# Kernel optimization log

Hardware: AMD Instinct MI355X
Metric: run time of the kernel (lower is better)

## Reference

```python
import jax, jax.numpy as jnp
from jax import lax
import numpy as np

STRIDE = 16.0
PRE_NMS_TOPN = 2000
POST_NMS_TOPN = 300
NMS_THRESH = 0.7
BBOX_XFORM_CLIP = float(np.log(1000.0 / 16.0))
NUM_ANCHORS = 15

# ---- Detectron generate_anchors (numpy, done once) ----

def _whctrs(a):
    w = a[2] - a[0] + 1.0
    h = a[3] - a[1] + 1.0
    return w, h, a[0] + 0.5 * (w - 1), a[1] + 0.5 * (h - 1)

def _mkanchors(ws, hs, xc, yc):
    ws = ws[:, None]; hs = hs[:, None]
    return np.hstack([xc - 0.5 * (ws - 1), yc - 0.5 * (hs - 1),
                      xc + 0.5 * (ws - 1), yc + 0.5 * (hs - 1)])

def _ratio_enum(anchor, ratios):
    w, h, xc, yc = _whctrs(anchor)
    size = w * h
    ws = np.round(np.sqrt(size / ratios))
    hs = np.round(ws * ratios)
    return _mkanchors(ws, hs, xc, yc)

def _scale_enum(anchor, scales):
    w, h, xc, yc = _whctrs(anchor)
    return _mkanchors(w * scales, h * scales, xc, yc)

def generate_anchors(stride, sizes, ratios):
    base = np.array([1, 1, stride, stride], dtype=np.float64) - 1
    ra = _ratio_enum(base, np.asarray(ratios, np.float64))
    anchors = np.vstack([_scale_enum(ra[i], np.asarray(sizes, np.float64) / stride)
                         for i in range(ra.shape[0])])
    return anchors.astype(np.float32)

ANCHORS_NP = generate_anchors(STRIDE, (32, 64, 128, 256, 512), (0.5, 1.0, 2.0))

# ---- proposal helpers (jax) ----

def decode_boxes(anchors, deltas):
    w = anchors[:, 2] - anchors[:, 0] + 1.0
    h = anchors[:, 3] - anchors[:, 1] + 1.0
    cx = anchors[:, 0] + 0.5 * w
    cy = anchors[:, 1] + 0.5 * h
    dx, dy = deltas[:, 0], deltas[:, 1]
    dw = jnp.minimum(deltas[:, 2], BBOX_XFORM_CLIP)
    dh = jnp.minimum(deltas[:, 3], BBOX_XFORM_CLIP)
    pcx = dx * w + cx
    pcy = dy * h + cy
    pw = jnp.exp(dw) * w
    ph = jnp.exp(dh) * h
    return jnp.stack([pcx - 0.5 * pw, pcy - 0.5 * ph,
                      pcx + 0.5 * pw - 1.0, pcy + 0.5 * ph - 1.0], axis=-1)

def clip_boxes(b, info):
    hmax = info[0] - 1.0
    wmax = info[1] - 1.0
    return jnp.stack([jnp.clip(b[:, 0], 0.0, wmax), jnp.clip(b[:, 1], 0.0, hmax),
                      jnp.clip(b[:, 2], 0.0, wmax), jnp.clip(b[:, 3], 0.0, hmax)], axis=-1)

def nms_keep(boxes):
    # boxes already sorted by descending score; greedy NMS via scan
    x1, y1, x2, y2 = boxes[:, 0], boxes[:, 1], boxes[:, 2], boxes[:, 3]
    areas = (x2 - x1 + 1.0) * (y2 - y1 + 1.0)
    xx1 = jnp.maximum(x1[:, None], x1[None, :])
    yy1 = jnp.maximum(y1[:, None], y1[None, :])
    xx2 = jnp.minimum(x2[:, None], x2[None, :])
    yy2 = jnp.minimum(y2[:, None], y2[None, :])
    inter = jnp.maximum(xx2 - xx1 + 1.0, 0.0) * jnp.maximum(yy2 - yy1 + 1.0, 0.0)
    iou = inter / (areas[:, None] + areas[None, :] - inter)
    K = boxes.shape[0]

    def body(keep, i):
        sup = jnp.any(keep & (iou[i] > NMS_THRESH))
        keep = keep.at[i].set(~sup)
        return keep, None

    keep, _ = lax.scan(body, jnp.zeros((K,), bool), jnp.arange(K))
    return keep


def setup_inputs() -> dict:
    key = jax.random.key(0)
    ks = jax.random.split(key, 4)
    x = jax.random.normal(ks[0], (2, 1024, 50, 84), jnp.float32)
    conv_w = 0.01 * jax.random.normal(ks[1], (1024, 1024, 3, 3), jnp.float32)
    conv_b = jnp.zeros((1024,), jnp.float32)
    cls_w = 0.01 * jax.random.normal(ks[2], (2 * NUM_ANCHORS, 1024, 1, 1), jnp.float32)
    cls_b = jnp.zeros((2 * NUM_ANCHORS,), jnp.float32)
    bbox_w = 0.01 * jax.random.normal(ks[3], (4 * NUM_ANCHORS, 1024, 1, 1), jnp.float32)
    bbox_b = jnp.zeros((4 * NUM_ANCHORS,), jnp.float32)
    im_info = jnp.array([[800.0, 1344.0, 1.0], [800.0, 1344.0, 1.0]], jnp.float32)
    return {"x": x, "conv_w": conv_w, "conv_b": conv_b, "cls_w": cls_w,
            "cls_b": cls_b, "bbox_w": bbox_w, "bbox_b": bbox_b, "im_info": im_info}


def reference(x, conv_w, conv_b, cls_w, cls_b, bbox_w, bbox_b, im_info):
    A = NUM_ANCHORS
    anchors = jnp.asarray(ANCHORS_NP)
    dn = ('NCHW', 'OIHW', 'NCHW')
    h = jax.nn.relu(lax.conv_general_dilated(x, conv_w, (1, 1), 'SAME',
                                             dimension_numbers=dn) + conv_b[None, :, None, None])
    cls_logits = lax.conv_general_dilated(h, cls_w, (1, 1), 'VALID',
                                          dimension_numbers=dn) + cls_b[None, :, None, None]
    bbox_pred = lax.conv_general_dilated(h, bbox_w, (1, 1), 'VALID',
                                         dimension_numbers=dn) + bbox_b[None, :, None, None]
    B, _, H, W = cls_logits.shape
    # softmax over the 2-way fg/bg axis, take fg prob: [B, A, H, W]
    prob = jax.nn.softmax(cls_logits.reshape(B, 2, A, H, W), axis=1)[:, 1]
    scores = prob.transpose(0, 2, 3, 1).reshape(B, -1)               # [B, H*W*A]
    deltas = bbox_pred.transpose(0, 2, 3, 1).reshape(B, H * W * A, 4)
    # shifted anchor grid, (h, w, a) flatten order matching Detectron
    sy = jnp.arange(H, dtype=jnp.float32) * STRIDE
    sx = jnp.arange(W, dtype=jnp.float32) * STRIDE
    ys, xs = jnp.meshgrid(sy, sx, indexing='ij')
    shifts = jnp.stack([xs, ys, xs, ys], axis=-1).reshape(-1, 4)      # [H*W, 4]
    all_anchors = (shifts[:, None, :] + anchors[None, :, :]).reshape(-1, 4)

    def per_image(sc, dl, info):
        boxes = clip_boxes(decode_boxes(all_anchors, dl), info)
        top_sc, idx = lax.top_k(sc, PRE_NMS_TOPN)
        top_boxes = boxes[idx]
        keep = nms_keep(top_boxes)
        order = jnp.argsort((~keep).astype(jnp.int32))[:POST_NMS_TOPN]  # kept first, score order
        valid = keep[order]
        out_boxes = jnp.where(valid[:, None], top_boxes[order], 0.0)
        out_sc = jnp.where(valid, top_sc[order], 0.0)
        return out_boxes, out_sc

    rois_b, probs_b = jax.vmap(per_image)(scores, deltas, im_info)
    batch_ids = jnp.repeat(jnp.arange(B, dtype=jnp.float32), POST_NMS_TOPN)
    rois = jnp.concatenate([batch_ids[:, None], rois_b.reshape(-1, 4)], axis=1)
    return cls_logits, bbox_pred, rois, probs_b.reshape(-1, 1)
```

## Files before the change

kernel.cpp:

```cpp
#include <hip/hip_runtime.h>
#include <math.h>

#define BATCH   2
#define CIN     1024
#define COUT    1024
#define HH      50
#define WW      84
#define HWX     4200
#define NA      15
#define NSC     63000
#define TOPN    2000
#define POSTN   300
#define CAP     8192
#define CLS_OFF   0
#define BBOX_OFF  252000
#define ROIS_OFF  756000
#define PROBS_OFF 759000

#define TPI 273
#define USTR 274

__constant__ double ANCH[NA][4] = {
  {-15.0,  -4.0,  30.0, 19.0},
  {-38.0, -16.0,  53.0, 31.0},
  {-84.0, -40.0,  99.0, 55.0},
  {-176.0,-88.0, 191.0,103.0},
  {-360.0,-184.0,375.0,199.0},
  {-8.0,  -8.0,  23.0, 23.0},
  {-24.0, -24.0, 39.0, 39.0},
  {-56.0, -56.0, 71.0, 71.0},
  {-120.0,-120.0,135.0,135.0},
  {-248.0,-248.0,263.0,263.0},
  {-3.0, -14.0, 18.0, 29.0},
  {-14.0, -36.0, 29.0, 51.0},
  {-36.0, -80.0, 51.0, 95.0},
  {-80.0,-168.0, 95.0,183.0},
  {-168.0,-344.0,183.0,359.0}
};

__constant__ double BTd[6][6] = {
  {4.0,  0.0, -5.0,  0.0, 1.0, 0.0},
  {0.0, -4.0, -4.0,  1.0, 1.0, 0.0},
  {0.0,  4.0, -4.0, -1.0, 1.0, 0.0},
  {0.0, -2.0, -1.0,  2.0, 1.0, 0.0},
  {0.0,  2.0, -1.0, -2.0, 1.0, 0.0},
  {0.0,  4.0,  0.0, -5.0, 0.0, 1.0}
};
__constant__ double ATd[4][6] = {
  {1.0, 1.0,  1.0, 1.0,  1.0, 0.0},
  {0.0, 1.0, -1.0, 2.0, -2.0, 0.0},
  {0.0, 1.0,  1.0, 4.0,  4.0, 0.0},
  {0.0, 1.0, -1.0, 8.0, -8.0, 1.0}
};

#define BBOX_CLIP 4.1351665567423560

#define WS_WT     0
#define WS_U      98304
#define WS_V      3465216
#define WS_C      16048128
#define WS_H64    19402752
#define OV_H      WS_V
#define OV_SC     (WS_C + 0)
#define OV_TIDX   (WS_C + 126000)
#define OV_TSC    (WS_C + 130000)
#define OV_BOX    (WS_C + 134000)
#define OV_MASK   (WS_C + 166000)

typedef double dx4 __attribute__((ext_vector_type(4)));

__device__ __forceinline__ void gload16(const void* gptr, void* lptr) {
  __builtin_amdgcn_global_load_lds(
      (const __attribute__((address_space(1))) unsigned int*)gptr,
      (__attribute__((address_space(3))) unsigned int*)lptr, 16, 0, 0);
}
#define MFMA64(a, b, c) __builtin_amdgcn_mfma_f64_16x16x4f64(a, b, c, 0, 0, 0)

__launch_bounds__(256)
__global__ void itrans_k(const float* __restrict__ x, double* __restrict__ U,
                         int b, int r) {
  __shared__ float XT[8][6][84];
  const int bx = blockIdx.x;
  const int cg  = bx & 127;
  const int ty  = bx >> 7;
  const int ci0 = cg * 8;
  for (int e = threadIdx.x; e < 4032; e += 256) {
    int ci = e / 504, rem = e % 504;
    int ry = rem / 84, xx = rem % 84;
    int y = ty*4 - 1 + ry;
    float v = 0.f;
    if (y >= 0 && y < HH) v = x[((size_t)(b*CIN + ci0 + ci)*HH + y)*WW + xx];
    XT[ci][ry][xx] = v;
  }
  __syncthreads();
  const int tid = threadIdx.x;
  if (tid < 168) {
    const int ci = tid / 21, tx = tid % 21;
    const double c0 = BTd[r][0], c1 = BTd[r][1], c2 = BTd[r][2];
    const double c3 = BTd[r][3], c4 = BTd[r][4], c5 = BTd[r][5];
    double tt[6];
#pragma unroll
    for (int j = 0; j < 6; ++j) {
      int col = tx*4 - 1 + j;
      double v = 0.0;
      if (col >= 0 && col < WW) {
        v = c0*(double)XT[ci][0][col] + c1*(double)XT[ci][1][col]
          + c2*(double)XT[ci][2][col] + c3*(double)XT[ci][3][col]
          + c4*(double)XT[ci][4][col] + c5*(double)XT[ci][5][col];
      }
      tt[j] = v;
    }
    const int t = ty*21 + tx;
#pragma unroll
    for (int c = 0; c < 6; ++c) {
      double u = BTd[c][0]*tt[0] + BTd[c][1]*tt[1] + BTd[c][2]*tt[2]
               + BTd[c][3]*tt[3] + BTd[c][4]*tt[4] + BTd[c][5]*tt[5];
      U[(size_t)(c*1024 + ci0 + ci)*USTR + t] = u;
    }
  }
}

#define GR0(a,b,c) (0.25*(a))
#define GR1(a,b,c) (-((a)+(b)+(c))*(1.0/6.0))
#define GR2(a,b,c) ((-(a)+(b)-(c))*(1.0/6.0))
#define GR3(a,b,c) (((a)+2.0*(b)+4.0*(c))*(1.0/24.0))
#define GR4(a,b,c) (((a)-2.0*(b)+4.0*(c))*(1.0/24.0))
#define GR5(a,b,c) ((c))
__launch_bounds__(256)
__global__ void wtrans_k(const float* __restrict__ conv_w, double* __restrict__ V,
                         int r) {
  const int g = blockIdx.x*256 + threadIdx.x;
  const int co = g & 1023, ci = g >> 10;
  const float* gp = conv_w + (size_t)(co*1024 + ci)*9;
  double g00 = (double)gp[0], g01 = (double)gp[1], g02 = (double)gp[2];
  double g10 = (double)gp[3], g11 = (double)gp[4], g12 = (double)gp[5];
  double g20 = (double)gp[6], g21 = (double)gp[7], g22 = (double)gp[8];
  double p0, p1, p2;
  switch (r) {
    case 0: p0=GR0(g00,g10,g20); p1=GR0(g01,g11,g21); p2=GR0(g02,g12,g22); break;
    case 1: p0=GR1(g00,g10,g20); p1=GR1(g01,g11,g21); p2=GR1(g02,g12,g22); break;
    case 2: p0=GR2(g00,g10,g20); p1=GR2(g01,g11,g21); p2=GR2(g02,g12,g22); break;
    case 3: p0=GR3(g00,g10,g20); p1=GR3(g01,g11,g21); p2=GR3(g02,g12,g22); break;
    case 4: p0=GR4(g00,g10,g20); p1=GR4(g01,g11,g21); p2=GR4(g02,g12,g22); break;
    default:p0=GR5(g00,g10,g20); p1=GR5(g01,g11,g21); p2=GR5(g02,g12,g22); break;
  }
  const size_t cico = (size_t)ci*1024 + co;
  V[0ull*1048576ull + cico] = GR0(p0,p1,p2);
  V[1ull*1048576ull + cico] = GR1(p0,p1,p2);
  V[2ull*1048576ull + cico] = GR2(p0,p1,p2);
  V[3ull*1048576ull + cico] = GR3(p0,p1,p2);
  V[4ull*1048576ull + cico] = GR4(p0,p1,p2);
  V[5ull*1048576ull + cico] = GR5(p0,p1,p2);
}

__launch_bounds__(256, 2)
__global__ void wgemm_k(const double* __restrict__ U, const double* __restrict__ V,
                        double* __restrict__ C) {
  __shared__ __align__(16) double As[2][32*64];
  __shared__ __align__(16) double Bs[2][32*64];
  const int tid = threadIdx.x;
  const int lane = tid & 63;
  const int w = tid >> 6;
  const int wm = w >> 1, wn = w & 1;
  const int l15 = lane & 15, lq = lane >> 4;
  const int bx = blockIdx.x;
  const int mt = bx >> 4, nt = bx & 15;
  const int t0 = mt * 64, n0 = nt * 64;
  const int z = blockIdx.z;
  const double* Ub = U + (size_t)z * (1024ull*USTR);
  const double* Vb = V + (size_t)z * 1048576ull;
  double* Cb = C + (size_t)z * ((size_t)TPI*1024);

  int pidx[4], nidx[4];
  {
    dx4 pr = {0.,0.,0.,0.}, pc = {0.,0.,0.,0.};
    pr = MFMA64((double)l15, 1.0, pr);
    pc = MFMA64(1.0, (double)l15, pc);
#pragma unroll
    for (int i = 0; i < 4; ++i) {
      pidx[i] = ((int)pr[i]) >> 2;
      nidx[i] = ((int)pc[i]) >> 2;
    }
  }

  auto stage = [&](int k0s, int slot) {
    char* Ad = (char*)&As[slot][0];
    char* Bd = (char*)&Bs[slot][0];
#pragma unroll
    for (int i = 0; i < 4; ++i) {
      int u = tid + i*256;
      int row = u >> 5, cp = u & 31;
      int t = t0 + 2*cp; if (t > 272) t = 272;
      gload16(Ub + (size_t)(k0s + row)*USTR + t, Ad + u*16);
    }
#pragma unroll
    for (int i = 0; i < 4; ++i) {
      int u = tid + i*256;
      int row = u >> 5, cp = u & 31;
      gload16(Vb + (size_t)(k0s + row)*1024 + n0 + 2*cp, Bd + u*16);
    }
  };

  dx4 acc[2][2];
#pragma unroll
  for (int i = 0; i < 2; ++i)
#pragma unroll
    for (int j = 0; j < 2; ++j) acc[i][j] = (dx4){0.,0.,0.,0.};

  stage(0, 0);
  __syncthreads();
  int cur = 0;
#pragma unroll 1
  for (int k0 = 0; k0 < 1024; k0 += 32) {
    if (k0 + 32 < 1024) stage(k0 + 32, cur ^ 1);
    const double* Ap = &As[cur][0];
    const double* Bp = &Bs[cur][0];
#pragma unroll
    for (int kk = 0; kk < 32; kk += 4) {
      const int ar = (kk + lq)*64 + wm*32 + l15;
      double a0 = Ap[ar], a1 = Ap[ar + 16];
      const int br = (kk + lq)*64 + wn*32 + l15;
      double b0 = Bp[br], b1 = Bp[br + 16];
      acc[0][0] = MFMA64(a0, b0, acc[0][0]);
      acc[0][1] = MFMA64(a0, b1, acc[0][1]);
      acc[1][0] = MFMA64(a1, b0, acc[1][0]);
      acc[1][1] = MFMA64(a1, b1, acc[1][1]);
    }
    __syncthreads();
    cur ^= 1;
  }

#pragma unroll
  for (int m2 = 0; m2 < 2; ++m2) {
#pragma unroll
    for (int n2 = 0; n2 < 2; ++n2) {
#pragma unroll
      for (int i = 0; i < 4; ++i) {
        int t = t0 + wm*32 + m2*16 + pidx[i];
        int co = n0 + wn*32 + n2*16 + nidx[i];
        if (t < TPI) Cb[(size_t)t*1024 + co] = acc[m2][n2][i];
      }
    }
  }
}

__launch_bounds__(256)
__global__ void otrans_k(const double* __restrict__ C, double* __restrict__ h64b,
                         int r) {
  const int g = blockIdx.x*256 + threadIdx.x;
  const int co = g & 1023, t = g >> 10;
  double m0 = C[((size_t)0*TPI + t)*1024 + co];
  double m1 = C[((size_t)1*TPI + t)*1024 + co];
  double m2 = C[((size_t)2*TPI + t)*1024 + co];
  double m3 = C[((size_t)3*TPI + t)*1024 + co];
  double m4 = C[((size_t)4*TPI + t)*1024 + co];
  double m5 = C[((size_t)5*TPI + t)*1024 + co];
  double s[4];
#pragma unroll
  for (int bb = 0; bb < 4; ++bb)
    s[bb] = ATd[bb][0]*m0 + ATd[bb][1]*m1 + ATd[bb][2]*m2
          + ATd[bb][3]*m3 + ATd[bb][4]*m4 + ATd[bb][5]*m5;
  const int ty = t / 21, tx = t % 21;
#pragma unroll
  for (int a = 0; a < 4; ++a) {
    const int y = ty*4 + a;
    if (y >= HH) continue;
    const double fa = ATd[a][r];
#pragma unroll
    for (int bb = 0; bb < 4; ++bb) {
      const size_t idx = ((size_t)(y*WW + tx*4 + bb))*1024 + co;
      if (r == 0) h64b[idx] = fa * s[bb];
      else        h64b[idx] += fa * s[bb];
    }
  }
}

__launch_bounds__(256)
__global__ void fin_k(const double* __restrict__ h64, const float* __restrict__ bias,
                      float* __restrict__ h) {
  __shared__ float T[64*65];
  const int m0  = blockIdx.x * 64;
  const int co0 = blockIdx.y * 64;
  const int b   = blockIdx.z;
  const int tid = threadIdx.x;
#pragma unroll
  for (int i = 0; i < 16; ++i) {
    int e = tid + i*256;
    int mi = e >> 6, coi = e & 63;
    int m = m0 + mi;
    double v = 0.0;
    if (m < HWX) v = h64[((size_t)b*HWX + m)*1024 + co0 + coi];
    T[mi*65 + coi] = (float)fmax(v + (double)bias[co0 + coi], 0.0);
  }
  __syncthreads();
#pragma unroll
  for (int i = 0; i < 16; ++i) {
    int e = tid + i*256;
    int coi = e >> 6, mi = e & 63;
    int m = m0 + mi;
    if (m < HWX) h[((size_t)(b*COUT + co0 + coi))*HWX + m] = T[mi*65 + coi];
  }
}

__global__ void wt_k(const float* __restrict__ cls_w, const float* __restrict__ bbox_w,
                     float* __restrict__ wT) {
  int t = blockIdx.x*256 + threadIdx.x;
  if (t >= 96*1024) return;
  int c = t / 96, o = t - (t/96)*96;
  float v = 0.f;
  if (o < 30)      v = cls_w[(size_t)o*1024 + c];
  else if (o < 90) v = bbox_w[(size_t)(o-30)*1024 + c];
  wT[t] = v;
}

__launch_bounds__(256, 2)
__global__ void heads_k(const float* __restrict__ h, const float* __restrict__ wT,
                        const float* __restrict__ cls_b, const float* __restrict__ bbox_b,
                        float* __restrict__ out_cls, float* __restrict__ out_bbox) {
  __shared__ __align__(16) float As[2][32*32];
  __shared__ __align__(16) float Bs[2][32*96];
  const int tid = threadIdx.x;
  const int lane = tid & 63;
  const int w = tid >> 6;
  const int wm = w >> 1, wn = w & 1;
  const int l15 = lane & 15, lq = lane >> 4;
  const int mt = blockIdx.x, b = blockIdx.y;
  const int m0 = mt * 32;

  int pidx[4], nidx[4];
  {
    dx4 pr = {0.,0.,0.,0.}, pc = {0.,0.,0.,0.};
    pr = MFMA64((double)l15, 1.0, pr);
    pc = MFMA64(1.0, (double)l15, pc);
#pragma unroll
    for (int i = 0; i < 4; ++i) {
      pidx[i] = ((int)pr[i]) >> 2;
      nidx[i] = ((int)pc[i]) >> 2;
    }
  }

  auto stage = [&](int c0, int slot) {
    {
      int row = tid >> 3, cp = tid & 7;
      int mm = m0 + cp*4; if (mm > HWX - 4) mm = HWX - 4;
      gload16(h + ((size_t)(b*COUT + c0 + row))*HWX + mm,
              (char*)&As[slot][0] + tid*16);
    }
#pragma unroll
    for (int i = 0; i < 3; ++i) {
      int e = tid + i*256;
      int row = e / 24, q = e % 24;
      gload16(wT + (size_t)(c0 + row)*96 + q*4,
              (char*)&Bs[slot][0] + e*16);
    }
  };

  dx4 acc[3];
#pragma unroll
  for (int j = 0; j < 3; ++j) acc[j] = (dx4){0.,0.,0.,0.};

  stage(0, 0);
  __syncthreads();
  int cur = 0;
#pragma unroll 1
  for (int c0 = 0; c0 < CIN; c0 += 32) {
    if (c0 + 32 < CIN) stage(c0 + 32, cur ^ 1);
    const float* Ap = &As[cur][0];
    const float* Bp = &Bs[cur][0];
#pragma unroll
    for (int kk = 0; kk < 32; kk += 4) {
      double a0 = (double)Ap[(kk + lq)*32 + wm*16 + l15];
      const int bb = (kk + lq)*96 + wn*48 + l15;
      double b0 = (double)Bp[bb];
      double b1 = (double)Bp[bb + 16];
      double b2 = (double)Bp[bb + 32];
      acc[0] = MFMA64(a0, b0, acc[0]);
      acc[1] = MFMA64(a0, b1, acc[1]);
      acc[2] = MFMA64(a0, b2, acc[2]);
    }
    __syncthreads();
    cur ^= 1;
  }

#pragma unroll
  for (int nf = 0; nf < 3; ++nf) {
#pragma unroll
    for (int i = 0; i < 4; ++i) {
      int m = m0 + wm*16 + pidx[i];
      int o = wn*48 + nf*16 + nidx[i];
      if (m < HWX) {
        if (o < 30) {
          out_cls[((size_t)(b*30 + o))*HWX + m] =
              (float)(acc[nf][i] + (double)cls_b[o]);
        } else if (o < 90) {
          out_bbox[((size_t)(b*60 + (o - 30)))*HWX + m] =
              (float)(acc[nf][i] + (double)bbox_b[o - 30]);
        }
      }
    }
  }
}

__global__ void score_k(const float* __restrict__ out_cls, float* __restrict__ scores) {
  int t = blockIdx.x*256 + threadIdx.x;
  if (t >= BATCH*NSC) return;
  int b = t / NSC; int r = t - b*NSC;
  int m = r / NA;  int a = r - m*NA;
  float l0 = out_cls[((size_t)(b*30 + a))*HWX + m];
  float l1 = out_cls[((size_t)(b*30 + a + NA))*HWX + m];
  double p = 1.0 / (1.0 + exp((double)l0 - (double)l1));
  scores[t] = (float)p;
}

__launch_bounds__(1024)
__global__ void topk_k(const float* __restrict__ scores,
                       unsigned* __restrict__ top_idx, float* __restrict__ top_score) {
  __shared__ unsigned hist[256];
  __shared__ unsigned sh_b1, sh_need, sh_cut, sh_cnt;
  __shared__ unsigned long long key[CAP];
  const int b = blockIdx.x;
  const int tid = threadIdx.x;
  const float* sc = scores + (size_t)b*NSC;

  if (tid < 256) hist[tid] = 0;
  __syncthreads();
  for (int i = tid; i < NSC; i += 1024) {
    unsigned k = __float_as_uint(sc[i]);
    atomicAdd(&hist[k >> 24], 1u);
  }
  __syncthreads();
  if (tid == 0) {
    unsigned cum = 0; int bin = 255;
    for (; bin >= 0; --bin) { cum += hist[bin]; if (cum >= TOPN) break; }
    sh_b1 = (unsigned)bin;
    sh_need = TOPN - (cum - hist[bin]);
  }
  __syncthreads();
  const unsigned b1 = sh_b1, need = sh_need;
  if (tid < 256) hist[tid] = 0;
  __syncthreads();
  for (int i = tid; i < NSC; i += 1024) {
    unsigned k = __float_as_uint(sc[i]);
    if ((k >> 24) == b1) atomicAdd(&hist[(k >> 16) & 255u], 1u);
  }
  __syncthreads();
  if (tid == 0) {
    unsigned cum = 0; int bin = 255;
    for (; bin >= 0; --bin) { cum += hist[bin]; if (cum >= need) break; }
    sh_cut = (b1 << 8) | (unsigned)bin;
    sh_cnt = 0;
  }
  __syncthreads();
  const unsigned cut = sh_cut;
  for (int i = tid; i < CAP; i += 1024) key[i] = 0ull;
  __syncthreads();
  for (int i = tid; i < NSC; i += 1024) {
    unsigned k = __float_as_uint(sc[i]);
    if ((k >> 16) >= cut) {
      unsigned p = atomicAdd(&sh_cnt, 1u);
      if (p < CAP)
        key[p] = ((unsigned long long)k << 32) | (unsigned long long)(0xFFFFFFFFu - (unsigned)i);
    }
  }
  __syncthreads();
  for (int k2 = 2; k2 <= CAP; k2 <<= 1) {
    for (int j = k2 >> 1; j > 0; j >>= 1) {
      for (int i = tid; i < CAP; i += 1024) {
        int p = i ^ j;
        if (p > i) {
          unsigned long long a = key[i], c = key[p];
          bool up = ((i & k2) == 0);
          if (up ? (a < c) : (a > c)) { key[i] = c; key[p] = a; }
        }
      }
      __syncthreads();
    }
  }
  for (int i = tid; i < TOPN; i += 1024) {
    unsigned long long kk = key[i];
    top_idx[(size_t)b*TOPN + i]   = 0xFFFFFFFFu - (unsigned)(kk & 0xFFFFFFFFull);
    top_score[(size_t)b*TOPN + i] = __uint_as_float((unsigned)(kk >> 32));
  }
}

__global__ void decode_k(const unsigned* __restrict__ top_idx,
                         const float* __restrict__ out_bbox,
                         const float* __restrict__ im_info,
                         double* __restrict__ boxesd) {
  int t = blockIdx.x*256 + threadIdx.x;
  if (t >= BATCH*TOPN) return;
  int b = t / TOPN;
  unsigned idx = top_idx[t];
  int a = idx % NA; int m = idx / NA;
  int yy = m / WW;  int xx = m - yy*WW;
  double sx = (double)xx * 16.0, sy = (double)yy * 16.0;
  double A0 = ANCH[a][0] + sx, A1 = ANCH[a][1] + sy;
  double A2 = ANCH[a][2] + sx, A3 = ANCH[a][3] + sy;
  double w_ = A2 - A0 + 1.0, h_ = A3 - A1 + 1.0;
  double cx = A0 + 0.5*w_,  cy = A1 + 0.5*h_;
  const float* bp = out_bbox + (size_t)b*60*HWX;
  double dx = (double)bp[(a*4+0)*HWX + m];
  double dy = (double)bp[(a*4+1)*HWX + m];
  double dw = fmin((double)bp[(a*4+2)*HWX + m], BBOX_CLIP);
  double dh = fmin((double)bp[(a*4+3)*HWX + m], BBOX_CLIP);
  double pcx = dx*w_ + cx, pcy = dy*h_ + cy;
  double pw = exp(dw)*w_,  ph = exp(dh)*h_;
  double x1 = pcx - 0.5*pw, y1 = pcy - 0.5*ph;
  double x2 = pcx + 0.5*pw - 1.0, y2 = pcy + 0.5*ph - 1.0;
  double hmax = (double)im_info[b*3+0] - 1.0;
  double wmax = (double)im_info[b*3+1] - 1.0;
  x1 = fmin(fmax(x1, 0.0), wmax); x2 = fmin(fmax(x2, 0.0), wmax);
  y1 = fmin(fmax(y1, 0.0), hmax); y2 = fmin(fmax(y2, 0.0), hmax);
  boxesd[(size_t)t*4+0] = x1; boxesd[(size_t)t*4+1] = y1;
  boxesd[(size_t)t*4+2] = x2; boxesd[(size_t)t*4+3] = y2;
}

__launch_bounds__(256)
__global__ void iou_k(const double* __restrict__ boxesd,
                      unsigned long long* __restrict__ mask) {
  __shared__ double BX[TOPN*4];
  const int b  = blockIdx.y;
  const int i0 = blockIdx.x * 8;
  const double* src = boxesd + (size_t)b*TOPN*4;
  for (int e = threadIdx.x; e < TOPN*4; e += 256) BX[e] = src[e];
  __syncthreads();
  const int il = threadIdx.x >> 5;
  const int w  = threadIdx.x & 31;
  const int i  = i0 + il;
  double x1 = BX[i*4+0], y1 = BX[i*4+1], x2 = BX[i*4+2], y2 = BX[i*4+3];
  double ai = (x2 - x1 + 1.0)*(y2 - y1 + 1.0);
  unsigned long long bits = 0ull;
  for (int jj = 0; jj < 64; ++jj) {
    int j = w*64 + jj;
    if (j >= TOPN) break;
    double bx1 = BX[j*4+0], by1 = BX[j*4+1], bx2 = BX[j*4+2], by2 = BX[j*4+3];
    double xx1 = fmax(x1, bx1), yy1 = fmax(y1, by1);
    double xx2 = fmin(x2, bx2), yy2 = fmin(y2, by2);
    double iw = fmax(xx2 - xx1 + 1.0, 0.0);
    double ih = fmax(yy2 - yy1 + 1.0, 0.0);
    double inter = iw * ih;
    double aj = (bx2 - bx1 + 1.0)*(by2 - by1 + 1.0);
    double iou = inter / (ai + aj - inter);
    if (iou > 0.7) bits |= (1ull << jj);
  }
  mask[((size_t)b*TOPN + i)*32 + w] = bits;
}

__launch_bounds__(256)
__global__ void nms_out_k(const unsigned long long* __restrict__ mask,
                          const double* __restrict__ boxesd,
                          const float* __restrict__ top_score,
                          float* __restrict__ rois, float* __restrict__ probs) {
  __shared__ unsigned long long MS[256*32];
  __shared__ int kept_idx[POSTN];
  __shared__ int s_cnt, s_done;
  const int b = blockIdx.x;
  const int tid = threadIdx.x;
  if (tid == 0) { s_done = 0; s_cnt = 0; }

  unsigned long long rem = 0ull;
  int cnt = 0;
  const int L = tid;

  for (int ch = 0; ch < 8; ++ch) {
    __syncthreads();
    if (s_done) break;
    const int base = ch * 256;
    for (int e = tid; e < 256*32; e += 256) {
      int row = base + (e >> 5);
      MS[e] = (row < TOPN) ? mask[((size_t)b*TOPN + row)*32 + (e & 31)] : 0ull;
    }
    __syncthreads();
    if (tid < 64) {
      const int lim = (base + 256 < TOPN) ? base + 256 : TOPN;
      int pos = base;
      while (true) {
        unsigned long long wmask = ~rem;
        int lo = pos - 64*L;
        if (lo >= 64) wmask = 0ull;
        else if (lo > 0) wmask &= (~0ull) << lo;
        int hi = lim - 64*L;
        if (hi <= 0) wmask = 0ull;
        else if (hi < 64) wmask &= ((1ull << hi) - 1ull);
        if (L >= 32) wmask = 0ull;
        unsigned long long bal = __ballot(wmask != 0ull);
        if (bal == 0ull) break;
        int lstar = __ffsll((long long)bal) - 1;
        int cand = 64*L + (wmask ? (__ffsll((long long)wmask) - 1) : 0);
        int i = __shfl(cand, lstar);
        if (L == 0) kept_idx[cnt] = i;
        ++cnt;
        if (cnt >= POSTN) {
          if (L == 0) { s_done = 1; }
          break;
        }
        if (L < 32) rem |= MS[(i - base)*32 + L];
        pos = i + 1;
      }
      if (L == 0) s_cnt = cnt;
    }
  }
  __syncthreads();
  const int n = s_cnt;

  for (int j = tid; j < POSTN; j += 256) {
    float* rr = rois + ((size_t)b*POSTN + j)*5;
    rr[0] = (float)b; rr[1] = 0.f; rr[2] = 0.f; rr[3] = 0.f; rr[4] = 0.f;
    probs[(size_t)b*POSTN + j] = 0.f;
  }
  for (int j = tid; j < n; j += 256) {
    int i = kept_idx[j];
    const double* bx = boxesd + ((size_t)b*TOPN + i)*4;
    float* rr = rois + ((size_t)b*POSTN + j)*5;
    rr[1] = (float)bx[0]; rr[2] = (float)bx[1];
    rr[3] = (float)bx[2]; rr[4] = (float)bx[3];
    probs[(size_t)b*POSTN + j] = top_score[(size_t)b*TOPN + i];
  }
}

extern "C" void kernel_launch(void* const* d_in, const int* in_sizes, int n_in,
                              void* d_out, int out_size, void* d_ws, size_t ws_size,
                              hipStream_t stream) {
  const float* x      = (const float*)d_in[0];
  const float* conv_w = (const float*)d_in[1];
  const float* conv_b = (const float*)d_in[2];
  const float* cls_w  = (const float*)d_in[3];
  const float* cls_b  = (const float*)d_in[4];
  const float* bbox_w = (const float*)d_in[5];
  const float* bbox_b = (const float*)d_in[6];
  const float* im_info= (const float*)d_in[7];

  float* out  = (float*)d_out;
  float* out_cls  = out + CLS_OFF;
  float* out_bbox = out + BBOX_OFF;
  float* rois     = out + ROIS_OFF;
  float* probs    = out + PROBS_OFF;

  float* wsf = (float*)d_ws;
  float*    wT      = wsf + WS_WT;
  double*   U       = (double*)(wsf + WS_U);
  double*   V       = (double*)(wsf + WS_V);
  double*   Cws     = (double*)(wsf + WS_C);
  double*   h64     = (double*)(wsf + WS_H64);
  float*    h       = wsf + OV_H;
  float*    scores  = wsf + OV_SC;
  unsigned* top_idx = (unsigned*)(wsf + OV_TIDX);
  float*    top_sc  = wsf + OV_TSC;
  double*   boxesd  = (double*)(wsf + OV_BOX);
  unsigned long long* mask = (unsigned long long*)(wsf + OV_MASK);

  wt_k<<<dim3((96*1024 + 255)/256), dim3(256), 0, stream>>>(cls_w, bbox_w, wT);
  for (int r = 0; r < 6; ++r) {
    wtrans_k<<<dim3(4096), dim3(256), 0, stream>>>(conv_w, V, r);
    for (int b = 0; b < 2; ++b) {
      itrans_k<<<dim3(1664), dim3(256), 0, stream>>>(x, U, b, r);
      wgemm_k<<<dim3(80, 1, 6), dim3(256), 0, stream>>>(U, V, Cws);
      otrans_k<<<dim3(1092), dim3(256), 0, stream>>>(Cws, h64 + (size_t)b*HWX*1024, r);
    }
  }
  fin_k<<<dim3(66, 16, 2), dim3(256), 0, stream>>>(h64, conv_b, h);
  heads_k<<<dim3(132, 2), dim3(256), 0, stream>>>(h, wT, cls_b, bbox_b, out_cls, out_bbox);
  score_k<<<dim3((BATCH*NSC + 255)/256), dim3(256), 0, stream>>>(out_cls, scores);
  topk_k<<<dim3(2), dim3(1024), 0, stream>>>(scores, top_idx, top_sc);
  decode_k<<<dim3((BATCH*TOPN + 255)/256), dim3(256), 0, stream>>>(top_idx, out_bbox, im_info, boxesd);
  iou_k<<<dim3(TOPN/8, 2), dim3(256), 0, stream>>>(boxesd, mask);
  nms_out_k<<<dim3(2), dim3(256), 0, stream>>>(mask, boxesd, top_sc, rois, probs);
}
```

Measured before the change: 1.898 ms.

## Add third radix pass, warp-aggregated atomics, and halve top-k sort buffer

The top-k kernel gains a third 8-bit radix-histogram pass so the candidate threshold is set at 24 bits. That makes the candidate set small enough to fit a 4096-entry bitonic sort instead of 8192. Histogram updates and the candidate compaction now use wave-level ballot aggregation, replacing per-thread shared atomics. The cost is one more pass over the scores and one more block barrier, in exchange for a sort with roughly half the compare-exchange steps. If more than 4096 scores ever tie on the top 24 bits, candidates overflow the buffer and are dropped.

```diff
diff --git a/kernel.cpp b/kernel.cpp
--- a/kernel.cpp
+++ b/kernel.cpp
@@ -11,7 +11,7 @@
 #define NSC     63000
 #define TOPN    2000
 #define POSTN   300
-#define CAP     8192
+#define CAP2    4096
 #define CLS_OFF   0
 #define BBOX_OFF  252000
 #define ROIS_OFF  756000
@@ -416,56 +416,104 @@
 __global__ void topk_k(const float* __restrict__ scores,
                        unsigned* __restrict__ top_idx, float* __restrict__ top_score) {
   __shared__ unsigned hist[256];
-  __shared__ unsigned sh_b1, sh_need, sh_cut, sh_cnt;
-  __shared__ unsigned long long key[CAP];
+  __shared__ unsigned sh_sel, sh_need, sh_cnt;
+  __shared__ unsigned long long key[CAP2];
   const int b = blockIdx.x;
   const int tid = threadIdx.x;
+  const int lane = tid & 63;
   const float* sc = scores + (size_t)b*NSC;
+  const int NIT = (NSC + 1023) / 1024;
+
+  auto whist = [&](bool act, unsigned bin) {
+    unsigned long long alive = __ballot(act);
+    while (alive) {
+      int leader = __ffsll((long long)alive) - 1;
+      unsigned lbin = __shfl(bin, leader);
+      unsigned long long match = __ballot(act && (bin == lbin));
+      if (lane == leader) atomicAdd(&hist[lbin], (unsigned)__popcll(match));
+      alive &= ~match;
+      act = act && (bin != lbin);
+    }
+  };
 
   if (tid < 256) hist[tid] = 0;
   __syncthreads();
-  for (int i = tid; i < NSC; i += 1024) {
-    unsigned k = __float_as_uint(sc[i]);
-    atomicAdd(&hist[k >> 24], 1u);
+  for (int it = 0; it < NIT; ++it) {
+    int i = tid + it*1024;
+    bool act = (i < NSC);
+    unsigned k = act ? __float_as_uint(sc[i]) : 0u;
+    whist(act, k >> 24);
   }
   __syncthreads();
   if (tid == 0) {
     unsigned cum = 0; int bin = 255;
     for (; bin >= 0; --bin) { cum += hist[bin]; if (cum >= TOPN) break; }
-    sh_b1 = (unsigned)bin;
+    sh_sel  = (unsigned)bin;
     sh_need = TOPN - (cum - hist[bin]);
   }
   __syncthreads();
-  const unsigned b1 = sh_b1, need = sh_need;
+  const unsigned b1 = sh_sel, need1 = sh_need;
+
   if (tid < 256) hist[tid] = 0;
   __syncthreads();
-  for (int i = tid; i < NSC; i += 1024) {
-    unsigned k = __float_as_uint(sc[i]);
-    if ((k >> 24) == b1) atomicAdd(&hist[(k >> 16) & 255u], 1u);
+  for (int it = 0; it < NIT; ++it) {
+    int i = tid + it*1024;
+    bool act = false; unsigned k = 0u;
+    if (i < NSC) { k = __float_as_uint(sc[i]); act = ((k >> 24) == b1); }
+    whist(act, (k >> 16) & 255u);
   }
   __syncthreads();
   if (tid == 0) {
     unsigned cum = 0; int bin = 255;
-    for (; bin >= 0; --bin) { cum += hist[bin]; if (cum >= need) break; }
-    sh_cut = (b1 << 8) | (unsigned)bin;
+    for (; bin >= 0; --bin) { cum += hist[bin]; if (cum >= need1) break; }
+    sh_sel  = (b1 << 8) | (unsigned)bin;
+    sh_need = need1 - (cum - hist[bin]);
+  }
+  __syncthreads();
+  const unsigned cut16 = sh_sel, need2 = sh_need;
+
+  if (tid < 256) hist[tid] = 0;
+  __syncthreads();
+  for (int it = 0; it < NIT; ++it) {
+    int i = tid + it*1024;
+    bool act = false; unsigned k = 0u;
+    if (i < NSC) { k = __float_as_uint(sc[i]); act = ((k >> 16) == cut16); }
+    whist(act, (k >> 8) & 255u);
+  }
+  __syncthreads();
+  if (tid == 0) {
+    unsigned cum = 0; int bin = 255;
+    for (; bin >= 0; --bin) { cum += hist[bin]; if (cum >= need2) break; }
+    sh_sel = (cut16 << 8) | (unsigned)bin;
     sh_cnt = 0;
   }
   __syncthreads();
-  const unsigned cut = sh_cut;
-  for (int i = tid; i < CAP; i += 1024) key[i] = 0ull;
-  __syncthreads();
-  for (int i = tid; i < NSC; i += 1024) {
-    unsigned k = __float_as_uint(sc[i]);
-    if ((k >> 16) >= cut) {
-      unsigned p = atomicAdd(&sh_cnt, 1u);
-      if (p < CAP)
-        key[p] = ((unsigned long long)k << 32) | (unsigned long long)(0xFFFFFFFFu - (unsigned)i);
-    }
-  }
-  __syncthreads();
-  for (int k2 = 2; k2 <= CAP; k2 <<= 1) {
+  const unsigned cut24 = sh_sel;
+
+  for (int i = tid; i < CAP2; i += 1024) key[i] = 0ull;
+  __syncthreads();
+  for (int it = 0; it < NIT; ++it) {
+    int i = tid + it*1024;
+    bool pred = false; unsigned k = 0u;
+    if (i < NSC) { k = __float_as_uint(sc[i]); pred = ((k >> 8) >= cut24); }
+    unsigned long long m = __ballot(pred);
+    if (m) {
+      int leader = __ffsll((long long)m) - 1;
+      unsigned base = 0;
+      if (lane == leader) base = atomicAdd(&sh_cnt, (unsigned)__popcll(m));
+      base = __shfl(base, leader);
+      if (pred) {
+        unsigned p = base + (unsigned)__popcll(m & ((1ull << lane) - 1ull));
+        if (p < CAP2)
+          key[p] = ((unsigned long long)k << 32) | (unsigned long long)(0xFFFFFFFFu - (unsigned)i);
+      }
+    }
+  }
+  __syncthreads();
+
+  for (int k2 = 2; k2 <= CAP2; k2 <<= 1) {
     for (int j = k2 >> 1; j > 0; j >>= 1) {
-      for (int i = tid; i < CAP; i += 1024) {
+      for (int i = tid; i < CAP2; i += 1024) {
         int p = i ^ j;
         if (p > i) {
           unsigned long long a = key[i], c = key[p];
```

Measured after the change: 2.047 ms. 7.8% more time.

## Split top-k radix select into multi-block histogram, cut, and compaction kernels

Applied to the files above, without the earlier changes.

The single two-block top-k kernel is replaced by a pipeline. A zeroing kernel clears global buffers, two grid-wide histogram passes each feed a scan-based cut kernel, and a wave-ballot compaction writes candidate keys to global memory. A separate two-block kernel then loads those keys into LDS and runs the existing bitonic sort. This spreads the scans over 63000 scores per image across many CUs and cuts per-element atomics to one per wavefront, at the cost of several extra kernel launches and a global round-trip for the keys.

```diff
diff --git a/kernel.cpp b/kernel.cpp
--- a/kernel.cpp
+++ b/kernel.cpp
@@ -11,7 +11,7 @@
 #define NSC     63000
 #define TOPN    2000
 #define POSTN   300
-#define CAP     8192
+#define CAPG    8192
 #define CLS_OFF   0
 #define BBOX_OFF  252000
 #define ROIS_OFF  756000
@@ -66,6 +66,13 @@
 #define OV_TSC    (WS_C + 130000)
 #define OV_BOX    (WS_C + 134000)
 #define OV_MASK   (WS_C + 166000)
+#define OV_GH     (WS_C + 422000)
+#define OV_GH2    (OV_GH  + 512)
+#define OV_GCA    (OV_GH2 + 512)
+#define OV_GCB    (OV_GCA + 16)
+#define OV_GCN    (OV_GCB + 16)
+#define OV_GK     (OV_GCN + 16)
+#define TZ_WORDS  (512 + 512 + 16 + 16 + 16 + 32768)
 
 typedef double dx4 __attribute__((ext_vector_type(4)));
 
@@ -412,60 +419,133 @@
   scores[t] = (float)p;
 }
 
+
+__global__ void tz_k(unsigned* __restrict__ gz) {
+  int t = blockIdx.x*256 + threadIdx.x;
+  if (t < TZ_WORDS) gz[t] = 0u;
+}
+
+__launch_bounds__(256)
+__global__ void histA_k(const float* __restrict__ scores, unsigned* __restrict__ ghist) {
+  __shared__ unsigned lh[256];
+  const int b = blockIdx.y;
+  const int base = blockIdx.x * 1024;
+  lh[threadIdx.x] = 0;
+  __syncthreads();
+  const float* sc = scores + (size_t)b*NSC;
+#pragma unroll
+  for (int q = 0; q < 4; ++q) {
+    int i = base + threadIdx.x + q*256;
+    if (i < NSC) atomicAdd(&lh[__float_as_uint(sc[i]) >> 24], 1u);
+  }
+  __syncthreads();
+  unsigned v = lh[threadIdx.x];
+  if (v) atomicAdd(&ghist[b*256 + threadIdx.x], v);
+}
+
+__launch_bounds__(256)
+__global__ void cutA_k(const unsigned* __restrict__ ghist, unsigned* __restrict__ gcutA) {
+  __shared__ unsigned s[256];
+  const int b = blockIdx.x;
+  const int t = threadIdx.x;
+  s[t] = ghist[b*256 + t];
+  __syncthreads();
+  for (int off = 1; off < 256; off <<= 1) {
+    unsigned v = (t + off < 256) ? s[t + off] : 0u;
+    __syncthreads();
+    s[t] += v;
+    __syncthreads();
+  }
+  unsigned cum  = s[t];
+  unsigned cum1 = (t < 255) ? s[t + 1] : 0u;
+  if (cum >= TOPN && (t == 255 || cum1 < TOPN))
+    gcutA[b] = ((unsigned)t << 16) | (TOPN - cum1);
+}
+
+__launch_bounds__(256)
+__global__ void histB_k(const float* __restrict__ scores, const unsigned* __restrict__ gcutA,
+                        unsigned* __restrict__ ghist2) {
+  __shared__ unsigned lh[256];
+  const int b = blockIdx.y;
+  const unsigned b1 = gcutA[b] >> 16;
+  const int base = blockIdx.x * 1024;
+  lh[threadIdx.x] = 0;
+  __syncthreads();
+  const float* sc = scores + (size_t)b*NSC;
+#pragma unroll
+  for (int q = 0; q < 4; ++q) {
+    int i = base + threadIdx.x + q*256;
+    if (i < NSC) {
+      unsigned k = __float_as_uint(sc[i]);
+      if ((k >> 24) == b1) atomicAdd(&lh[(k >> 16) & 255u], 1u);
+    }
+  }
+  __syncthreads();
+  unsigned v = lh[threadIdx.x];
+  if (v) atomicAdd(&ghist2[b*256 + threadIdx.x], v);
+}
+
+__launch_bounds__(256)
+__global__ void cutB_k(const unsigned* __restrict__ ghist2, const unsigned* __restrict__ gcutA,
+                       unsigned* __restrict__ gcutB) {
+  __shared__ unsigned s[256];
+  const int b = blockIdx.x;
+  const int t = threadIdx.x;
+  const unsigned b1 = gcutA[b] >> 16, need = gcutA[b] & 0xFFFFu;
+  s[t] = ghist2[b*256 + t];
+  __syncthreads();
+  for (int off = 1; off < 256; off <<= 1) {
+    unsigned v = (t + off < 256) ? s[t + off] : 0u;
+    __syncthreads();
+    s[t] += v;
+    __syncthreads();
+  }
+  unsigned cum  = s[t];
+  unsigned cum1 = (t < 255) ? s[t + 1] : 0u;
+  if (cum >= need && (t == 255 || cum1 < need))
+    gcutB[b] = (b1 << 8) | (unsigned)t;
+}
+
+__launch_bounds__(256)
+__global__ void compact_k(const float* __restrict__ scores, const unsigned* __restrict__ gcutB,
+                          unsigned long long* __restrict__ gkeys, unsigned* __restrict__ gcnt) {
+  const int b = blockIdx.y;
+  const unsigned cut = gcutB[b];
+  const int base = blockIdx.x * 1024;
+  const int lane = threadIdx.x & 63;
+  const float* sc = scores + (size_t)b*NSC;
+#pragma unroll
+  for (int q = 0; q < 4; ++q) {
+    int i = base + threadIdx.x + q*256;
+    bool pred = false; unsigned k = 0u;
+    if (i < NSC) { k = __float_as_uint(sc[i]); pred = ((k >> 16) >= cut); }
+    unsigned long long m = __ballot(pred);
+    if (m) {
+      int leader = __ffsll((long long)m) - 1;
+      unsigned bp = 0;
+      if (lane == leader) bp = atomicAdd(&gcnt[b], (unsigned)__popcll(m));
+      bp = __shfl(bp, leader);
+      if (pred) {
+        unsigned p = bp + (unsigned)__popcll(m & ((1ull << lane) - 1ull));
+        if (p < CAPG)
+          gkeys[(size_t)b*CAPG + p] =
+              ((unsigned long long)k << 32) | (unsigned long long)(0xFFFFFFFFu - (unsigned)i);
+      }
+    }
+  }
+}
+
 __launch_bounds__(1024)
-__global__ void topk_k(const float* __restrict__ scores,
-                       unsigned* __restrict__ top_idx, float* __restrict__ top_score) {
-  __shared__ unsigned hist[256];
-  __shared__ unsigned sh_b1, sh_need, sh_cut, sh_cnt;
-  __shared__ unsigned long long key[CAP];
+__global__ void sortk_k(const unsigned long long* __restrict__ gkeys,
+                        unsigned* __restrict__ top_idx, float* __restrict__ top_score) {
+  __shared__ unsigned long long key[CAPG];
   const int b = blockIdx.x;
   const int tid = threadIdx.x;
-  const float* sc = scores + (size_t)b*NSC;
-
-  if (tid < 256) hist[tid] = 0;
-  __syncthreads();
-  for (int i = tid; i < NSC; i += 1024) {
-    unsigned k = __float_as_uint(sc[i]);
-    atomicAdd(&hist[k >> 24], 1u);
-  }
-  __syncthreads();
-  if (tid == 0) {
-    unsigned cum = 0; int bin = 255;
-    for (; bin >= 0; --bin) { cum += hist[bin]; if (cum >= TOPN) break; }
-    sh_b1 = (unsigned)bin;
-    sh_need = TOPN - (cum - hist[bin]);
-  }
-  __syncthreads();
-  const unsigned b1 = sh_b1, need = sh_need;
-  if (tid < 256) hist[tid] = 0;
-  __syncthreads();
-  for (int i = tid; i < NSC; i += 1024) {
-    unsigned k = __float_as_uint(sc[i]);
-    if ((k >> 24) == b1) atomicAdd(&hist[(k >> 16) & 255u], 1u);
-  }
-  __syncthreads();
-  if (tid == 0) {
-    unsigned cum = 0; int bin = 255;
-    for (; bin >= 0; --bin) { cum += hist[bin]; if (cum >= need) break; }
-    sh_cut = (b1 << 8) | (unsigned)bin;
-    sh_cnt = 0;
-  }
-  __syncthreads();
-  const unsigned cut = sh_cut;
-  for (int i = tid; i < CAP; i += 1024) key[i] = 0ull;
-  __syncthreads();
-  for (int i = tid; i < NSC; i += 1024) {
-    unsigned k = __float_as_uint(sc[i]);
-    if ((k >> 16) >= cut) {
-      unsigned p = atomicAdd(&sh_cnt, 1u);
-      if (p < CAP)
-        key[p] = ((unsigned long long)k << 32) | (unsigned long long)(0xFFFFFFFFu - (unsigned)i);
-    }
-  }
-  __syncthreads();
-  for (int k2 = 2; k2 <= CAP; k2 <<= 1) {
+  for (int i = tid; i < CAPG; i += 1024) key[i] = gkeys[(size_t)b*CAPG + i];
+  __syncthreads();
+  for (int k2 = 2; k2 <= CAPG; k2 <<= 1) {
     for (int j = k2 >> 1; j > 0; j >>= 1) {
-      for (int i = tid; i < CAP; i += 1024) {
+      for (int i = tid; i < CAPG; i += 1024) {
         int p = i ^ j;
         if (p > i) {
           unsigned long long a = key[i], c = key[p];
@@ -648,6 +728,12 @@
   float*    top_sc  = wsf + OV_TSC;
   double*   boxesd  = (double*)(wsf + OV_BOX);
   unsigned long long* mask = (unsigned long long*)(wsf + OV_MASK);
+  unsigned* ghist   = (unsigned*)(wsf + OV_GH);
+  unsigned* ghist2  = (unsigned*)(wsf + OV_GH2);
+  unsigned* gcutA   = (unsigned*)(wsf + OV_GCA);
+  unsigned* gcutB   = (unsigned*)(wsf + OV_GCB);
+  unsigned* gcnt    = (unsigned*)(wsf + OV_GCN);
+  unsigned long long* gkeys = (unsigned long long*)(wsf + OV_GK);
 
   wt_k<<<dim3((96*1024 + 255)/256), dim3(256), 0, stream>>>(cls_w, bbox_w, wT);
   for (int r = 0; r < 6; ++r) {
@@ -660,8 +746,14 @@
   }
   fin_k<<<dim3(66, 16, 2), dim3(256), 0, stream>>>(h64, conv_b, h);
   heads_k<<<dim3(132, 2), dim3(256), 0, stream>>>(h, wT, cls_b, bbox_b, out_cls, out_bbox);
+  tz_k<<<dim3((TZ_WORDS + 255)/256), dim3(256), 0, stream>>>(ghist);
   score_k<<<dim3((BATCH*NSC + 255)/256), dim3(256), 0, stream>>>(out_cls, scores);
-  topk_k<<<dim3(2), dim3(1024), 0, stream>>>(scores, top_idx, top_sc);
+  histA_k<<<dim3(62, 2), dim3(256), 0, stream>>>(scores, ghist);
+  cutA_k<<<dim3(2), dim3(256), 0, stream>>>(ghist, gcutA);
+  histB_k<<<dim3(62, 2), dim3(256), 0, stream>>>(scores, gcutA, ghist2);
+  cutB_k<<<dim3(2), dim3(256), 0, stream>>>(ghist2, gcutA, gcutB);
+  compact_k<<<dim3(62, 2), dim3(256), 0, stream>>>(scores, gcutB, gkeys, gcnt);
+  sortk_k<<<dim3(2), dim3(1024), 0, stream>>>(gkeys, top_idx, top_sc);
   decode_k<<<dim3((BATCH*TOPN + 255)/256), dim3(256), 0, stream>>>(top_idx, out_bbox, im_info, boxesd);
   iou_k<<<dim3(TOPN/8, 2), dim3(256), 0, stream>>>(boxesd, mask);
   nms_out_k<<<dim3(2), dim3(256), 0, stream>>>(mask, boxesd, top_sc, rois, probs);
```

New measurement: 1.877 ms. No clear change (-1.1%).
